# Kernel optimization log

Hardware: AMD Instinct MI355X
Metric: run time of the kernel (lower is better)

The kernel has to match this reference:

```python
import jax, jax.numpy as jnp
import numpy as np

SCORE_WEIGHT = 0.5
MAX_ITER = 20
PROJ_ITER = 5
RELAX_LR = 0.1
EPS = 1e-8

P, D, T, O, H, W = 256, 256, 2, 24, 240, 432


def setup_inputs() -> dict:
    key = jax.random.key(0)
    k1, k2, k3, k4, k5 = jax.random.split(key, 5)
    proposed_feature = jax.random.normal(k1, (P, D), dtype=jnp.float32)
    proposed_mask = (jax.random.uniform(k2, (P, H, W)) > 0.7).astype(jnp.float32)
    template_feature = jax.random.normal(k3, (T, O, D), dtype=jnp.float32)
    mask_last_occurence = (jax.random.uniform(k4, (O, H, W)) > 0.7).astype(jnp.float32)
    proposal_score = jax.random.uniform(k5, (P,), dtype=jnp.float32)
    return {
        "proposed_feature": proposed_feature,
        "proposed_mask": proposed_mask,
        "template_feature": template_feature,
        "mask_last_occurence": mask_last_occurence,
        "proposal_score": proposal_score,
    }


def relax_matching(C, max_iter=MAX_ITER, proj_iter=PROJ_INNER if False else PROJ_ITER, lr=RELAX_LR):
    """Projected-gradient relaxation of the assignment LP.
    Gradient step on <C, X>, then proj_iter alternating projections onto
    {X >= 0, X <= 1, row sums == 1}. Returns mean of iterates (sum(X_list)/len)."""
    K, N = C.shape
    X0 = jnp.full((K, N), 1.0 / N, dtype=C.dtype)

    def project(X):
        def body(_, X):
            X = jnp.clip(X, 0.0, 1.0)
            X = X / (jnp.sum(X, axis=1, keepdims=True) + EPS)
            return X
        return jax.lax.fori_loop(0, proj_iter, body, X)

    def step(X, _):
        X = project(X - lr * C)
        return X, X

    _, Xs = jax.lax.scan(step, X0, None, length=max_iter)
    return jnp.mean(Xs, axis=0)  # [K, N]


def reference(proposed_feature, proposed_mask, template_feature,
              mask_last_occurence, proposal_score):
    n_prop = proposed_mask.shape[0]
    n_tplt = mask_last_occurence.shape[0]
    h, w = proposed_mask.shape[1], proposed_mask.shape[2]

    # --- feature cosine similarity, averaged over template frames ---
    kf = proposed_feature / (jnp.linalg.norm(proposed_feature, axis=1, keepdims=True) + EPS)
    qf = template_feature / (jnp.linalg.norm(template_feature, axis=2, keepdims=True) + EPS)
    feature_sim = jnp.einsum('tod,pd->op', qf, kf) / template_feature.shape[0]  # [O, P]

    # --- pairwise binary-mask IoU without materializing [O*P, HW] ---
    A = mask_last_occurence.reshape(n_tplt, -1)  # [O, HW] templates
    B = proposed_mask.reshape(n_prop, -1)        # [P, HW] proposals
    inter = A @ B.T                              # [O, P]
    union = A.sum(axis=1)[:, None] + B.sum(axis=1)[None, :] - inter
    iou = inter / (union + EPS)

    sim_matrix = feature_sim * (1.0 - SCORE_WEIGHT) + iou * SCORE_WEIGHT
    # P > O so no padding branch; cost is [O, P]
    cost_matrix = -sim_matrix

    Ridx = relax_matching(cost_matrix)           # averaged iterates, [O, P]
    # training branch (is_test == 0)
    logic_mask = (Ridx > 0.01).astype(Ridx.dtype)
    binX = Ridx * logic_mask

    full_outmask = (binX @ B).reshape(n_tplt, h, w)                 # [O, H, W]
    match_score = jnp.max(jnp.clip(Ridx, 0.0, 1.0) * -cost_matrix, axis=1)  # [O]
    det_score = jnp.sum(proposal_score[None, :] * binX, axis=1)     # [O]
    return (full_outmask, match_score, det_score)
```

## Files before the change

kernel.cpp:

```cpp
#include <hip/hip_runtime.h>

#define HW 103680
#define WORDS 1620
#define NGRP 405
#define NP 256
#define NO 24
#define ND 256
#define EPSF 1e-8f
#define OUTM (NO*HW)

typedef unsigned long long u64;

__device__ __forceinline__ float waveRedSum(float v) {
  v += __int_as_float(__builtin_amdgcn_update_dpp(0, __float_as_int(v), 0x111, 0xf, 0xf, false));
  v += __int_as_float(__builtin_amdgcn_update_dpp(0, __float_as_int(v), 0x112, 0xf, 0xf, false));
  v += __int_as_float(__builtin_amdgcn_update_dpp(0, __float_as_int(v), 0x114, 0xf, 0xf, false));
  v += __int_as_float(__builtin_amdgcn_update_dpp(0, __float_as_int(v), 0x118, 0xf, 0xf, false));
  v += __int_as_float(__builtin_amdgcn_update_dpp(0, __float_as_int(v), 0x142, 0xf, 0xf, false));
  v += __int_as_float(__builtin_amdgcn_update_dpp(0, __float_as_int(v), 0x143, 0xf, 0xf, false));
  return __int_as_float(__builtin_amdgcn_readlane(__float_as_int(v), 63));
}
__device__ __forceinline__ float waveRedMax(float v) {
  int vi = __float_as_int(v);
  v = fmaxf(v, __int_as_float(__builtin_amdgcn_update_dpp(vi, vi, 0x111, 0xf, 0xf, false))); vi = __float_as_int(v);
  v = fmaxf(v, __int_as_float(__builtin_amdgcn_update_dpp(vi, vi, 0x112, 0xf, 0xf, false))); vi = __float_as_int(v);
  v = fmaxf(v, __int_as_float(__builtin_amdgcn_update_dpp(vi, vi, 0x114, 0xf, 0xf, false))); vi = __float_as_int(v);
  v = fmaxf(v, __int_as_float(__builtin_amdgcn_update_dpp(vi, vi, 0x118, 0xf, 0xf, false))); vi = __float_as_int(v);
  v = fmaxf(v, __int_as_float(__builtin_amdgcn_update_dpp(vi, vi, 0x142, 0xf, 0xf, false))); vi = __float_as_int(v);
  v = fmaxf(v, __int_as_float(__builtin_amdgcn_update_dpp(vi, vi, 0x143, 0xf, 0xf, false)));
  return __int_as_float(__builtin_amdgcn_readlane(__float_as_int(v), 63));
}

__global__ __launch_bounds__(256) void pack_kernel(const float* __restrict__ pm,
                                                   const float* __restrict__ ml,
                                                   u64* __restrict__ bbits,
                                                   u64* __restrict__ abits) {
  int row = blockIdx.y;
  int wir = (blockIdx.x * 256 + threadIdx.x) >> 6;
  int lane = threadIdx.x & 63;
  const float* rp;
  u64* bits;
  if (row < NP) { rp = pm + (size_t)row * HW;        bits = bbits + (size_t)row * WORDS; }
  else          { rp = ml + (size_t)(row - NP) * HW; bits = abits + (size_t)(row - NP) * WORDS; }
  for (int g = wir; g < NGRP; g += 28) {
    float4 v = *(const float4*)(rp + g * 256 + lane * 4);
    u64 m0 = __ballot(v.x != 0.0f);
    u64 m1 = __ballot(v.y != 0.0f);
    u64 m2 = __ballot(v.z != 0.0f);
    u64 m3 = __ballot(v.w != 0.0f);
    if (lane == 0) {
      ulonglong2 s0; s0.x = m0; s0.y = m1;
      ulonglong2 s1; s1.x = m2; s1.y = m3;
      *(ulonglong2*)(bits + g * 4)     = s0;
      *(ulonglong2*)(bits + g * 4 + 2) = s1;
    }
  }
}

__global__ __launch_bounds__(256) void interfeat_kernel(const u64* __restrict__ ab,
                                                        const u64* __restrict__ bb,
                                                        const float* __restrict__ pf,
                                                        const float* __restrict__ tf,
                                                        float* __restrict__ C) {
  int wid = (blockIdx.x * 256 + threadIdx.x) >> 6;
  int lane = threadIdx.x & 63;
  int o = wid >> 8, p = wid & 255;
  const u64* ar = ab + (size_t)o * WORDS;
  const u64* br = bb + (size_t)p * WORDS;
  int cnt = 0, ucnt = 0;
  for (int w = lane; w < WORDS; w += 64) {
    u64 a = ar[w], b = br[w];
    cnt  += (int)__popcll(a & b);
    ucnt += (int)__popcll(a | b);
  }
  float inter = waveRedSum((float)cnt);
  float uni   = waveRedSum((float)ucnt);
  float4 f = *(const float4*)(pf + p * ND + lane * 4);
  float4 a = *(const float4*)(tf + o * ND + lane * 4);
  float4 b = *(const float4*)(tf + (NO + o) * ND + lane * 4);
  float nf = waveRedSum(f.x*f.x + f.y*f.y + f.z*f.z + f.w*f.w);
  float na = waveRedSum(a.x*a.x + a.y*a.y + a.z*a.z + a.w*a.w);
  float nb = waveRedSum(b.x*b.x + b.y*b.y + b.z*b.z + b.w*b.w);
  float d0 = waveRedSum(a.x*f.x + a.y*f.y + a.z*f.z + a.w*f.w);
  float d1 = waveRedSum(b.x*f.x + b.y*f.y + b.z*f.z + b.w*f.w);
  if (lane == 0) {
    float invf = 1.0f / (sqrtf(nf) + EPSF);
    float inva = 1.0f / (sqrtf(na) + EPSF);
    float invb = 1.0f / (sqrtf(nb) + EPSF);
    float fs  = (d0 * inva + d1 * invb) * invf * 0.5f;
    float iou = inter / (uni + EPSF);
    C[wid] = -(fs * 0.5f + iou * 0.5f);
  }
}

__global__ __launch_bounds__(64) void solve_kernel(const float* __restrict__ Cm,
                                                   const float* __restrict__ score,
                                                   int* __restrict__ nzidx,
                                                   float* __restrict__ nzval,
                                                   int* __restrict__ nzcnt,
                                                   float* __restrict__ out) {
  int o = blockIdx.x, lane = threadIdx.x;
  float4 c4 = *(const float4*)(Cm + o * NP + lane * 4);
  float C[4] = {c4.x, c4.y, c4.z, c4.w};
  float sim[4], X[4], Xs[4];
#pragma unroll
  for (int j = 0; j < 4; ++j) {
    sim[j] = -C[j];
    X[j] = 1.0f / 256.0f;
    Xs[j] = 0.0f;
  }
  for (int it = 0; it < 20; ++it) {
#pragma unroll
    for (int j = 0; j < 4; ++j) X[j] = X[j] - 0.1f * C[j];
    for (int k = 0; k < 5; ++k) {
#pragma unroll
      for (int j = 0; j < 4; ++j) X[j] = fminf(fmaxf(X[j], 0.0f), 1.0f);
      float s = waveRedSum((X[0] + X[1]) + (X[2] + X[3]));
#pragma unroll
      for (int j = 0; j < 4; ++j) X[j] = X[j] / (s + EPSF);
    }
#pragma unroll
    for (int j = 0; j < 4; ++j) Xs[j] += X[j];
  }
  float R[4], bx[4];
#pragma unroll
  for (int j = 0; j < 4; ++j) {
    R[j] = Xs[j] / 20.0f;
    bx[j] = (R[j] > 0.01f) ? R[j] : 0.0f;
  }
  unsigned long long lt = (1ull << lane) - 1ull;
  int base = 0;
#pragma unroll
  for (int j = 0; j < 4; ++j) {
    unsigned long long m = __ballot(bx[j] != 0.0f);
    if (bx[j] != 0.0f) {
      int pos = base + (int)__popcll(m & lt);
      nzidx[o * NP + pos] = lane * 4 + j;
      nzval[o * NP + pos] = bx[j];
    }
    base += (int)__popcll(m);
  }
  if (lane == 0) nzcnt[o] = base;
  float mv = -1e30f;
#pragma unroll
  for (int j = 0; j < 4; ++j)
    mv = fmaxf(mv, fminf(fmaxf(R[j], 0.0f), 1.0f) * sim[j]);
  mv = waveRedMax(mv);
  float4 sc4 = *(const float4*)(score + lane * 4);
  float dv = waveRedSum(((sc4.x * bx[0]) + (sc4.y * bx[1])) + ((sc4.z * bx[2]) + (sc4.w * bx[3])));
  if (lane == 0) { out[OUTM + o] = mv; out[OUTM + NO + o] = dv; }
}

__global__ __launch_bounds__(256) void outmask_kernel(const float* __restrict__ pm,
                                                      const int* __restrict__ nzidx,
                                                      const float* __restrict__ nzval,
                                                      const int* __restrict__ nzcnt,
                                                      float* __restrict__ out) {
  int o = blockIdx.y;
  int t = blockIdx.x * 256 + threadIdx.x;
  int hw4 = t * 4;
  if (hw4 >= HW) return;
  int cnt = nzcnt[o];
  float4 acc = make_float4(0.0f, 0.0f, 0.0f, 0.0f);
  for (int i = 0; i < cnt; ++i) {
    int p = nzidx[o * NP + i];
    float v = nzval[o * NP + i];
    float4 m = *(const float4*)(pm + (size_t)p * HW + hw4);
    acc.x = fmaf(v, m.x, acc.x);
    acc.y = fmaf(v, m.y, acc.y);
    acc.z = fmaf(v, m.z, acc.z);
    acc.w = fmaf(v, m.w, acc.w);
  }
  *(float4*)(out + (size_t)o * HW + hw4) = acc;
}

extern "C" void kernel_launch(void* const* d_in, const int* in_sizes, int n_in,
                              void* d_out, int out_size, void* d_ws, size_t ws_size,
                              hipStream_t stream) {
  const float* pf = (const float*)d_in[0];
  const float* pm = (const float*)d_in[1];
  const float* tf = (const float*)d_in[2];
  const float* ml = (const float*)d_in[3];
  const float* sc = (const float*)d_in[4];
  float* out = (float*)d_out;
  char* ws = (char*)d_ws;

  u64*   bbits = (u64*)(ws);
  u64*   abits = (u64*)(ws + 3317760);
  int*   nzidx = (int*)(ws + 3317760);
  float* nzval = (float*)(ws + 3317760 + 24576);
  int*   nzcnt = (int*)(ws + 3317760 + 49152);
  float* Cm    = (float*)(ws + 3631136);

  hipLaunchKernelGGL(pack_kernel,      dim3(7, 280), dim3(256), 0, stream, pm, ml, bbits, abits);
  hipLaunchKernelGGL(interfeat_kernel, dim3(1536),   dim3(256), 0, stream, abits, bbits, pf, tf, Cm);
  hipLaunchKernelGGL(solve_kernel,     dim3(24),     dim3(64),  0, stream, Cm, sc,
                     nzidx, nzval, nzcnt, out);
  hipLaunchKernelGGL(outmask_kernel,   dim3(102, 24), dim3(256), 0, stream, pm, nzidx, nzval, nzcnt, out);
}
```

Measured before the change: 57.19 us.

## Build output mask from packed bitmasks and unroll pack and popcount loops

The output-mask kernel now rebuilds each proposal's contribution from the 1-bit packed masks made in the pack stage, instead of re-reading the full float masks. This cuts the gather traffic per selected proposal by roughly 32x, but it relies on mask values being exactly 0 or 1. The pack loop is also manually unrolled by two so that two loads are in flight per iteration. The IoU popcount loop uses a fixed trip count with an unroll pragma and a separate tail.

```diff
diff --git a/kernel.cpp b/kernel.cpp
--- a/kernel.cpp
+++ b/kernel.cpp
@@ -29,6 +29,21 @@
   v = fmaxf(v, __int_as_float(__builtin_amdgcn_update_dpp(vi, vi, 0x142, 0xf, 0xf, false))); vi = __float_as_int(v);
   v = fmaxf(v, __int_as_float(__builtin_amdgcn_update_dpp(vi, vi, 0x143, 0xf, 0xf, false)));
   return __int_as_float(__builtin_amdgcn_readlane(__float_as_int(v), 63));
+}
+
+__device__ __forceinline__ void pack_group(const float* __restrict__ rp,
+                                           u64* __restrict__ bits,
+                                           int g, int lane, float4 v) {
+  u64 m0 = __ballot(v.x != 0.0f);
+  u64 m1 = __ballot(v.y != 0.0f);
+  u64 m2 = __ballot(v.z != 0.0f);
+  u64 m3 = __ballot(v.w != 0.0f);
+  if (lane == 0) {
+    ulonglong2 s0; s0.x = m0; s0.y = m1;
+    ulonglong2 s1; s1.x = m2; s1.y = m3;
+    *(ulonglong2*)(bits + g * 4)     = s0;
+    *(ulonglong2*)(bits + g * 4 + 2) = s1;
+  }
 }
 
 __global__ __launch_bounds__(256) void pack_kernel(const float* __restrict__ pm,
@@ -42,18 +57,17 @@
   u64* bits;
   if (row < NP) { rp = pm + (size_t)row * HW;        bits = bbits + (size_t)row * WORDS; }
   else          { rp = ml + (size_t)(row - NP) * HW; bits = abits + (size_t)(row - NP) * WORDS; }
-  for (int g = wir; g < NGRP; g += 28) {
-    float4 v = *(const float4*)(rp + g * 256 + lane * 4);
-    u64 m0 = __ballot(v.x != 0.0f);
-    u64 m1 = __ballot(v.y != 0.0f);
-    u64 m2 = __ballot(v.z != 0.0f);
-    u64 m3 = __ballot(v.w != 0.0f);
-    if (lane == 0) {
-      ulonglong2 s0; s0.x = m0; s0.y = m1;
-      ulonglong2 s1; s1.x = m2; s1.y = m3;
-      *(ulonglong2*)(bits + g * 4)     = s0;
-      *(ulonglong2*)(bits + g * 4 + 2) = s1;
-    }
+  int g = wir;
+  while (g + 28 < NGRP) {
+    float4 v0 = *(const float4*)(rp + g * 256 + lane * 4);
+    float4 v1 = *(const float4*)(rp + (g + 28) * 256 + lane * 4);
+    pack_group(rp, bits, g, lane, v0);
+    pack_group(rp, bits, g + 28, lane, v1);
+    g += 56;
+  }
+  if (g < NGRP) {
+    float4 v0 = *(const float4*)(rp + g * 256 + lane * 4);
+    pack_group(rp, bits, g, lane, v0);
   }
 }
 
@@ -65,19 +79,25 @@
   int wid = (blockIdx.x * 256 + threadIdx.x) >> 6;
   int lane = threadIdx.x & 63;
   int o = wid >> 8, p = wid & 255;
-  const u64* ar = ab + (size_t)o * WORDS;
-  const u64* br = bb + (size_t)p * WORDS;
-  int cnt = 0, ucnt = 0;
-  for (int w = lane; w < WORDS; w += 64) {
-    u64 a = ar[w], b = br[w];
-    cnt  += (int)__popcll(a & b);
-    ucnt += (int)__popcll(a | b);
-  }
-  float inter = waveRedSum((float)cnt);
-  float uni   = waveRedSum((float)ucnt);
   float4 f = *(const float4*)(pf + p * ND + lane * 4);
   float4 a = *(const float4*)(tf + o * ND + lane * 4);
   float4 b = *(const float4*)(tf + (NO + o) * ND + lane * 4);
+  const u64* arl = ab + (size_t)o * WORDS + lane;
+  const u64* brl = bb + (size_t)p * WORDS + lane;
+  int cnt = 0, ucnt = 0;
+#pragma unroll 5
+  for (int k = 0; k < 25; ++k) {
+    u64 av = arl[k * 64], bv = brl[k * 64];
+    cnt  += (int)__popcll(av & bv);
+    ucnt += (int)__popcll(av | bv);
+  }
+  if (lane < WORDS - 1600) {
+    u64 av = arl[1600], bv = brl[1600];
+    cnt  += (int)__popcll(av & bv);
+    ucnt += (int)__popcll(av | bv);
+  }
+  float inter = waveRedSum((float)cnt);
+  float uni   = waveRedSum((float)ucnt);
   float nf = waveRedSum(f.x*f.x + f.y*f.y + f.z*f.z + f.w*f.w);
   float na = waveRedSum(a.x*a.x + a.y*a.y + a.z*a.z + a.w*a.w);
   float nb = waveRedSum(b.x*b.x + b.y*b.y + b.z*b.z + b.w*b.w);
@@ -151,27 +171,28 @@
   if (lane == 0) { out[OUTM + o] = mv; out[OUTM + NO + o] = dv; }
 }
 
-__global__ __launch_bounds__(256) void outmask_kernel(const float* __restrict__ pm,
+__global__ __launch_bounds__(256) void outmask_kernel(const u64* __restrict__ bb,
                                                       const int* __restrict__ nzidx,
                                                       const float* __restrict__ nzval,
                                                       const int* __restrict__ nzcnt,
                                                       float* __restrict__ out) {
   int o = blockIdx.y;
-  int t = blockIdx.x * 256 + threadIdx.x;
-  int hw4 = t * 4;
-  if (hw4 >= HW) return;
+  int g = blockIdx.x * 4 + (threadIdx.x >> 6);
+  int lane = threadIdx.x & 63;
+  if (g >= NGRP) return;
   int cnt = nzcnt[o];
-  float4 acc = make_float4(0.0f, 0.0f, 0.0f, 0.0f);
+  float ax = 0.0f, ay = 0.0f, az = 0.0f, aw = 0.0f;
   for (int i = 0; i < cnt; ++i) {
-    int p = nzidx[o * NP + i];
+    int p   = nzidx[o * NP + i];
     float v = nzval[o * NP + i];
-    float4 m = *(const float4*)(pm + (size_t)p * HW + hw4);
-    acc.x = fmaf(v, m.x, acc.x);
-    acc.y = fmaf(v, m.y, acc.y);
-    acc.z = fmaf(v, m.z, acc.z);
-    acc.w = fmaf(v, m.w, acc.w);
-  }
-  *(float4*)(out + (size_t)o * HW + hw4) = acc;
+    const u64* wp = bb + (size_t)p * WORDS + g * 4;
+    u64 m0 = wp[0], m1 = wp[1], m2 = wp[2], m3 = wp[3];
+    ax += ((m0 >> lane) & 1ull) ? v : 0.0f;
+    ay += ((m1 >> lane) & 1ull) ? v : 0.0f;
+    az += ((m2 >> lane) & 1ull) ? v : 0.0f;
+    aw += ((m3 >> lane) & 1ull) ? v : 0.0f;
+  }
+  *(float4*)(out + (size_t)o * HW + g * 256 + lane * 4) = make_float4(ax, ay, az, aw);
 }
 
 extern "C" void kernel_launch(void* const* d_in, const int* in_sizes, int n_in,
@@ -192,9 +213,9 @@
   int*   nzcnt = (int*)(ws + 3317760 + 49152);
   float* Cm    = (float*)(ws + 3631136);
 
-  hipLaunchKernelGGL(pack_kernel,      dim3(7, 280), dim3(256), 0, stream, pm, ml, bbits, abits);
-  hipLaunchKernelGGL(interfeat_kernel, dim3(1536),   dim3(256), 0, stream, abits, bbits, pf, tf, Cm);
-  hipLaunchKernelGGL(solve_kernel,     dim3(24),     dim3(64),  0, stream, Cm, sc,
+  hipLaunchKernelGGL(pack_kernel,      dim3(7, 280),  dim3(256), 0, stream, pm, ml, bbits, abits);
+  hipLaunchKernelGGL(interfeat_kernel, dim3(1536),    dim3(256), 0, stream, abits, bbits, pf, tf, Cm);
+  hipLaunchKernelGGL(solve_kernel,     dim3(24),      dim3(64),  0, stream, Cm, sc,
                      nzidx, nzval, nzcnt, out);
-  hipLaunchKernelGGL(outmask_kernel,   dim3(102, 24), dim3(256), 0, stream, pm, nzidx, nzval, nzcnt, out);
-}
+  hipLaunchKernelGGL(outmask_kernel,   dim3(102, 24), dim3(256), 0, stream, bbits, nzidx, nzval, nzcnt, out);
+}
```

Measured after the change: 55.97 us. -2.1%, faster.
